# Performance work log

Measured on AMD Instinct MI355X. Metric: run time of the kernel, lower is better.

The kernel has to match this reference:

```python
import jax, jax.numpy as jnp
import numpy as np

KNOW, ITEM, D, L, LAT, B, S = 1024, 20000, 128, 2, 256, 256, 200
NTOT = ITEM + KNOW
E1, E2 = 32768, 160000


def graph_layer(h, W, a, src, dst, n):
    # GAT-style: gather src/dst, edge MLP, segment softmax over dst, weighted scatter-sum
    z = h @ W                                              # [N, D]
    e = jax.nn.leaky_relu((jnp.concatenate([z[src], z[dst]], axis=-1) @ a)[:, 0])  # [E]
    m = jax.ops.segment_max(e, dst, num_segments=n)
    m = jnp.where(jnp.isfinite(m), m, 0.0)                 # nodes with no in-edges
    w = jnp.exp(e - m[dst])                                # [E]
    den = jax.ops.segment_sum(w, dst, num_segments=n)      # [N]
    num = jax.ops.segment_sum(w[:, None] * z[src], dst, num_segments=n)  # [N, D]
    return jnp.where(den[:, None] > 0, num / jnp.maximum(den, 1e-12)[:, None], 0.0)


def setup_inputs() -> dict:
    key = jax.random.key(0)
    ks = jax.random.split(key, 32)
    p = lambda i, shp: jax.random.normal(ks[i], shp, dtype=jnp.float32) * 0.05
    inp = {
        'p_rec': jax.random.randint(ks[0], (B, S), 0, ITEM),
        'p_target': jax.random.randint(ks[1], (B,), 0, S),
        'a_rec': jax.random.randint(ks[2], (B, S), 0, 3),
        'kn_rec': jax.random.uniform(ks[3], (B, S, KNOW), dtype=jnp.float32),
        'kn_num': jnp.ones((B, S), dtype=jnp.float32),
        'src1': jax.random.randint(ks[4], (E1,), 0, KNOW),
        'dst1': jax.random.randint(ks[5], (E1,), 0, KNOW),
        'src2': jax.random.randint(ks[6], (E2,), 0, NTOT),
        'dst2': jax.random.randint(ks[7], (E2,), 0, NTOT),
        'src3': jax.random.randint(ks[8], (E2,), 0, NTOT),
        'dst3': jax.random.randint(ks[9], (E2,), 0, NTOT),
        'kn_table': p(10, (KNOW, D)),
        'exer_table': p(11, (ITEM, D)),
        'ans_table': p(12, (3, D)),
        'gW': p(13, (L, 3, D, D)),
        'gA': p(14, (L, 3, 2 * D, 1)),
        'raW1': p(15, (L, D, D)),
        'raB1': jnp.zeros((L, D), jnp.float32),
        'raW2': p(16, (L, D, 1)),
        'actW1': p(17, (3 * D, LAT)),
        'actB1': jnp.zeros((LAT,), jnp.float32),
        'actW2': p(18, (LAT, ITEM)),
        'actB2': jnp.zeros((ITEM,), jnp.float32),
        'vW1': p(19, (3, 3 * D, LAT)),
        'vB1': jnp.zeros((3, LAT), jnp.float32),
        'vW2': p(20, (3, LAT, 1)),
        'vB2': jnp.zeros((3, 1), jnp.float32),
    }
    return inp


def reference(p_rec, p_target, a_rec, kn_rec, kn_num, src1, dst1, src2, dst2, src3, dst3,
              kn_table, exer_table, ans_table, gW, gA, raW1, raB1, raW2,
              actW1, actB1, actW2, actB2, vW1, vB1, vW2, vB2):
    kn, ex = kn_table, exer_table
    for l in range(L):  # GraphEncoder: stacked Fusion blocks (distinct params)
        k_dir = graph_layer(kn, gW[l, 0], gA[l, 0], src1, dst1, KNOW)
        ek = jnp.concatenate([ex, kn], axis=0)             # [NTOT, D]
        kfe = graph_layer(ek, gW[l, 1], gA[l, 1], src2, dst2, NTOT)
        efk = graph_layer(ek, gW[l, 2], gA[l, 2], src3, dst3, NTOT)
        A_, B_ = k_dir, kfe[ITEM:]
        ra = lambda x: jnp.tanh(x @ raW1[l] + raB1[l]) @ raW2[l]  # [KNOW, 1]
        s = jax.nn.softmax(jnp.concatenate([ra(A_), ra(B_)], axis=1), axis=1)
        kn = s[:, :1] * A_ + s[:, 1:2] * B_
        ex = efk[:ITEM]
    # hidden_layer
    be = ex[p_rec]                                         # [B, S, D]
    ba = ans_table[a_rec]                                  # [B, S, D]
    bk = jnp.einsum('bsk,kd->bsd', kn_rec, kn) / kn_num[..., None]
    item = jnp.concatenate([be, ba, bk], axis=-1)          # [B, S, 3D]
    m = (jnp.arange(S)[None, :] < (p_target + 1)[:, None]).astype(item.dtype)
    h = (item * m[..., None]).sum(axis=1) / m.sum(axis=1, keepdims=True)  # [B, 3D]
    logits = jnp.tanh(h @ actW1 + actB1) @ actW2 + actB2   # [B, ITEM]
    vh = jnp.tanh(jnp.einsum('bd,kdl->kbl', h, vW1) + vB1[:, None, :])
    vals = jnp.einsum('kbl,klo->kbo', vh, vW2) + vB2[:, None, :]  # [3, B, 1]
    return logits, vals[0], vals[1], vals[2]
```

## Files before the change

kernel.cpp:

```cpp
#include <hip/hip_runtime.h>

#define D 128
#define KNOW 1024
#define ITEM 20000
#define NTOT (ITEM + KNOW)
#define LAYERS 2
#define LAT 256
#define BB 256
#define SS 200
#define H3 (3 * D)
#define CH 4
#define ZROWS 64
#define NBK (KNOW / ZROWS)
#define NBN ((NTOT + ZROWS - 1) / ZROWS)
#define NAGG (KNOW + KNOW + NTOT)
#define XPITCH 68

__global__ __launch_bounds__(256) void zdv(
    const float* __restrict__ Xe, const float* __restrict__ Xk,
    const float* __restrict__ gW, const float* __restrict__ gA, int layer,
    float* __restrict__ z1, float* __restrict__ z2, float* __restrict__ z3,
    float* __restrict__ ds1, float* __restrict__ dd1,
    float* __restrict__ ds2, float* __restrict__ dd2,
    float* __restrict__ ds3, float* __restrict__ dd3)
{
    __shared__ __align__(16) float xT[D * XPITCH];
    int bid = blockIdx.x;
    int g, row0, nmax;
    if (bid < NBK)            { g = 0; row0 = bid * ZROWS;                nmax = KNOW; }
    else if (bid < NBK + NBN) { g = 1; row0 = (bid - NBK) * ZROWS;        nmax = NTOT; }
    else                      { g = 2; row0 = (bid - NBK - NBN) * ZROWS;  nmax = NTOT; }
    const float* W = gW + (size_t)(layer * 3 + g) * D * D;
    const float* A = gA + (size_t)(layer * 3 + g) * 2 * D;
    float* Z  = (g == 0) ? z1  : (g == 1 ? z2  : z3);
    float* DS = (g == 0) ? ds1 : (g == 1 ? ds2 : ds3);
    float* DD = (g == 0) ? dd1 : (g == 1 ? dd2 : dd3);

    int tid = threadIdx.x;
#pragma unroll
    for (int i = 0; i < 8; ++i) {
        int flat = tid + i * 256;
        int row  = flat >> 5;
        int f4   = flat & 31;
        int grow = row0 + row;
        float4 v = make_float4(0.f, 0.f, 0.f, 0.f);
        if (grow < nmax) {
            const float* src = (g == 0) ? (Xk + (size_t)grow * D)
                             : (grow < ITEM ? Xe + (size_t)grow * D
                                            : Xk + (size_t)(grow - ITEM) * D);
            v = *(const float4*)(src + f4 * 4);
        }
        int slot = row ^ ((f4 & 7) << 2);
        int kk = f4 * 4;
        xT[(kk + 0) * XPITCH + slot] = v.x;
        xT[(kk + 1) * XPITCH + slot] = v.y;
        xT[(kk + 2) * XPITCH + slot] = v.z;
        xT[(kk + 3) * XPITCH + slot] = v.w;
    }
    __syncthreads();

    int cg = tid & 31;
    int rg = tid >> 5;
    int c0 = cg * 4;
    int r0a = rg * 8, r0b = rg * 8 + 4;

    float acc[8][4];
#pragma unroll
    for (int r = 0; r < 8; ++r)
#pragma unroll
        for (int c = 0; c < 4; ++c) acc[r][c] = 0.f;

#pragma unroll 4
    for (int k = 0; k < D; ++k) {
        float4 wv = *(const float4*)(W + (size_t)k * D + c0);
        int xc = ((k >> 2) & 7) << 2;
        float4 xa = *(const float4*)&xT[k * XPITCH + (r0a ^ xc)];
        float4 xb = *(const float4*)&xT[k * XPITCH + (r0b ^ xc)];
        acc[0][0] = fmaf(xa.x, wv.x, acc[0][0]); acc[0][1] = fmaf(xa.x, wv.y, acc[0][1]);
        acc[0][2] = fmaf(xa.x, wv.z, acc[0][2]); acc[0][3] = fmaf(xa.x, wv.w, acc[0][3]);
        acc[1][0] = fmaf(xa.y, wv.x, acc[1][0]); acc[1][1] = fmaf(xa.y, wv.y, acc[1][1]);
        acc[1][2] = fmaf(xa.y, wv.z, acc[1][2]); acc[1][3] = fmaf(xa.y, wv.w, acc[1][3]);
        acc[2][0] = fmaf(xa.z, wv.x, acc[2][0]); acc[2][1] = fmaf(xa.z, wv.y, acc[2][1]);
        acc[2][2] = fmaf(xa.z, wv.z, acc[2][2]); acc[2][3] = fmaf(xa.z, wv.w, acc[2][3]);
        acc[3][0] = fmaf(xa.w, wv.x, acc[3][0]); acc[3][1] = fmaf(xa.w, wv.y, acc[3][1]);
        acc[3][2] = fmaf(xa.w, wv.z, acc[3][2]); acc[3][3] = fmaf(xa.w, wv.w, acc[3][3]);
        acc[4][0] = fmaf(xb.x, wv.x, acc[4][0]); acc[4][1] = fmaf(xb.x, wv.y, acc[4][1]);
        acc[4][2] = fmaf(xb.x, wv.z, acc[4][2]); acc[4][3] = fmaf(xb.x, wv.w, acc[4][3]);
        acc[5][0] = fmaf(xb.y, wv.x, acc[5][0]); acc[5][1] = fmaf(xb.y, wv.y, acc[5][1]);
        acc[5][2] = fmaf(xb.y, wv.z, acc[5][2]); acc[5][3] = fmaf(xb.y, wv.w, acc[5][3]);
        acc[6][0] = fmaf(xb.z, wv.x, acc[6][0]); acc[6][1] = fmaf(xb.z, wv.y, acc[6][1]);
        acc[6][2] = fmaf(xb.z, wv.z, acc[6][2]); acc[6][3] = fmaf(xb.z, wv.w, acc[6][3]);
        acc[7][0] = fmaf(xb.w, wv.x, acc[7][0]); acc[7][1] = fmaf(xb.w, wv.y, acc[7][1]);
        acc[7][2] = fmaf(xb.w, wv.z, acc[7][2]); acc[7][3] = fmaf(xb.w, wv.w, acc[7][3]);
    }

#pragma unroll
    for (int r = 0; r < 8; ++r) {
        int grow = row0 + ((r < 4) ? (r0a + r) : (r0b + r - 4));
        if (grow < nmax) {
            float4 v = make_float4(acc[r][0], acc[r][1], acc[r][2], acc[r][3]);
            *(float4*)(Z + (size_t)grow * D + c0) = v;
        }
    }

    float4 as = *(const float4*)(A + c0);
    float4 ad = *(const float4*)(A + D + c0);
    float ps[8], pd[8];
#pragma unroll
    for (int r = 0; r < 8; ++r) {
        ps[r] = acc[r][0] * as.x + acc[r][1] * as.y + acc[r][2] * as.z + acc[r][3] * as.w;
        pd[r] = acc[r][0] * ad.x + acc[r][1] * ad.y + acc[r][2] * ad.z + acc[r][3] * ad.w;
    }
#pragma unroll
    for (int m = 16; m; m >>= 1) {
#pragma unroll
        for (int r = 0; r < 8; ++r) {
            ps[r] += __shfl_xor(ps[r], m, 64);
            pd[r] += __shfl_xor(pd[r], m, 64);
        }
    }
    if (cg == 0) {
#pragma unroll
        for (int r = 0; r < 8; ++r) {
            int grow = row0 + ((r < 4) ? (r0a + r) : (r0b + r - 4));
            if (grow < nmax) { DS[grow] = ps[r]; DD[grow] = pd[r]; }
        }
    }
}

__global__ void hist3(const int* __restrict__ d1, const int* __restrict__ d2, const int* __restrict__ d3,
                      int E1, int E2, int* __restrict__ c1, int* __restrict__ c2, int* __restrict__ c3) {
    int i = blockIdx.x * blockDim.x + threadIdx.x;
    if (i < E1) atomicAdd(&c1[d1[i]], 1);
    else if (i < E1 + E2) { int d = d2[i - E1]; if (d >= ITEM) atomicAdd(&c2[d - ITEM], 1); }
    else if (i < E1 + 2 * E2) atomicAdd(&c3[d3[i - E1 - E2]], 1);
}

__global__ __launch_bounds__(1024) void exscan3(int* __restrict__ c1, int* __restrict__ o1,
                                                int* __restrict__ c2, int* __restrict__ o2,
                                                int* __restrict__ c3, int* __restrict__ o3) {
    int g = blockIdx.x;
    int* cnt = (g == 0) ? c1 : (g == 1 ? c2 : c3);
    int* off = (g == 0) ? o1 : (g == 1 ? o2 : o3);
    int n = (g == 2) ? NTOT : KNOW;
    __shared__ int wsum[16];
    __shared__ int carry;
    int tid = threadIdx.x, lane = tid & 63, wid = tid >> 6;
    if (tid == 0) { carry = 0; off[0] = 0; }
    __syncthreads();
    for (int base = 0; base < n; base += 1024) {
        int i = base + tid;
        int v = (i < n) ? cnt[i] : 0;
        int x = v;
#pragma unroll
        for (int d = 1; d < 64; d <<= 1) { int t = __shfl_up(x, d, 64); x += (lane >= d) ? t : 0; }
        if (lane == 63) wsum[wid] = x;
        __syncthreads();
        if (wid == 0) {
            int w = (lane < 16) ? wsum[lane] : 0;
#pragma unroll
            for (int d = 1; d < 16; d <<= 1) { int t = __shfl_up(w, d, 64); w += (lane >= d) ? t : 0; }
            if (lane < 16) wsum[lane] = w;
        }
        __syncthreads();
        int incl = x + ((wid > 0) ? wsum[wid - 1] : 0) + carry;
        if (i < n) { off[i + 1] = incl; cnt[i] = incl - v; }
        __syncthreads();
        if (tid == 1023) carry = incl;
        __syncthreads();
    }
}

__global__ void scatter3(const int* __restrict__ s1, const int* __restrict__ d1,
                         const int* __restrict__ s2, const int* __restrict__ d2,
                         const int* __restrict__ s3, const int* __restrict__ d3,
                         int E1, int E2, int* __restrict__ cur1, int* __restrict__ cur2, int* __restrict__ cur3,
                         int* __restrict__ e1, int* __restrict__ e2, int* __restrict__ e3) {
    int i = blockIdx.x * blockDim.x + threadIdx.x;
    if (i < E1) { int p = atomicAdd(&cur1[d1[i]], 1); e1[p] = s1[i]; }
    else if (i < E1 + E2) { int j = i - E1; int d = d2[j]; if (d >= ITEM) { int p = atomicAdd(&cur2[d - ITEM], 1); e2[p] = s2[j]; } }
    else if (i < E1 + 2 * E2) { int j = i - E1 - E2; int p = atomicAdd(&cur3[d3[j]], 1); e3[p] = s3[j]; }
}

__global__ __launch_bounds__(256) void agg3(
    const float* __restrict__ z1, const float* __restrict__ z2, const float* __restrict__ z3,
    const float* __restrict__ ds1, const float* __restrict__ dd1,
    const float* __restrict__ ds2, const float* __restrict__ dd2,
    const float* __restrict__ ds3, const float* __restrict__ dd3,
    const int* __restrict__ off1, const int* __restrict__ es1,
    const int* __restrict__ off2, const int* __restrict__ es2,
    const int* __restrict__ off3, const int* __restrict__ es3,
    float* __restrict__ kdir, float* __restrict__ kfe_kn, float* __restrict__ nxt)
{
    int u = blockIdx.x * 4 + (threadIdx.x >> 6);
    int lane = threadIdx.x & 63;
    if (u >= NAGG) return;
    const float* Z; const float* dsrc; const int* off; const int* es; float* out; float dd; int row;
    if (u < KNOW)          { row = u;            Z = z1; dsrc = ds1; off = off1; es = es1; out = kdir   + (size_t)row * D; dd = dd1[row]; }
    else if (u < 2 * KNOW) { row = u - KNOW;     Z = z2; dsrc = ds2; off = off2; es = es2; out = kfe_kn + (size_t)row * D; dd = dd2[ITEM + row]; }
    else                   { row = u - 2 * KNOW; Z = z3; dsrc = ds3; off = off3; es = es3; out = nxt    + (size_t)row * D; dd = dd3[row]; }
    int e0 = off[row], e1 = off[row + 1];
    float2 res = make_float2(0.f, 0.f);
    if (e1 > e0) {
        float mx = -3.4e38f;
        for (int e = e0 + lane; e < e1; e += 64) {
            float t = dsrc[es[e]] + dd;
            t = (t > 0.f) ? t : 0.01f * t;
            mx = fmaxf(mx, t);
        }
#pragma unroll
        for (int o = 32; o; o >>= 1) mx = fmaxf(mx, __shfl_xor(mx, o, 64));
        float den = 0.f, ax = 0.f, ay = 0.f;
        for (int e = e0; e < e1; ++e) {
            int s = es[e];
            float t = dsrc[s] + dd;
            t = (t > 0.f) ? t : 0.01f * t;
            float w = expf(t - mx);
            den += w;
            float2 zv = ((const float2*)(Z + (size_t)s * D))[lane];
            ax += w * zv.x; ay += w * zv.y;
        }
        float inv = 1.f / fmaxf(den, 1e-12f);
        res = make_float2(ax * inv, ay * inv);
    }
    ((float2*)out)[lane] = res;
}

__global__ __launch_bounds__(128) void combine(const float* __restrict__ kdir, const float* __restrict__ kfe_kn,
                                               const float* __restrict__ raW1, const float* __restrict__ raB1,
                                               const float* __restrict__ raW2, float* __restrict__ out) {
    __shared__ float A[D], Bv[D];
    __shared__ float2 red[128];
    int i = blockIdx.x, j = threadIdx.x;
    A[j]  = kdir[(size_t)i * D + j];
    Bv[j] = kfe_kn[(size_t)i * D + j];
    __syncthreads();
    float accA = raB1[j], accB = accA;
    for (int k = 0; k < D; ++k) {
        float w = raW1[k * D + j];
        accA = fmaf(A[k], w, accA);
        accB = fmaf(Bv[k], w, accB);
    }
    float w2 = raW2[j];
    float pA = tanhf(accA) * w2, pB = tanhf(accB) * w2;
    red[j] = make_float2(pA, pB);
    __syncthreads();
    for (int st = 64; st > 0; st >>= 1) {
        if (j < st) { red[j].x += red[j + st].x; red[j].y += red[j + st].y; }
        __syncthreads();
    }
    float rA = red[0].x, rB = red[0].y;
    float mx = fmaxf(rA, rB);
    float eA = expf(rA - mx), eB = expf(rB - mx), s = 1.f / (eA + eB);
    out[(size_t)(ITEM + i) * D + j] = (eA * s) * A[j] + (eB * s) * Bv[j];
}

__global__ __launch_bounds__(256) void krowk(const float* __restrict__ kn_rec, const float* __restrict__ kn_num,
                                             const int* __restrict__ p_target, float* __restrict__ krowP) {
    int b = blockIdx.x, ch = blockIdx.y;
    int cnt = p_target[b] + 1;
    int per = (SS + CH - 1) / CH;
    int s0 = ch * per, s1 = s0 + per;
    if (s1 > cnt) s1 = cnt;
    int k0 = threadIdx.x * 4;
    float4 a = make_float4(0.f, 0.f, 0.f, 0.f);
    for (int s = s0; s < s1; ++s) {
        float inv = 1.f / kn_num[b * SS + s];
        float4 v = *(const float4*)(kn_rec + ((size_t)b * SS + s) * KNOW + k0);
        a.x += v.x * inv; a.y += v.y * inv; a.z += v.z * inv; a.w += v.w * inv;
    }
    *(float4*)(krowP + ((size_t)ch * BB + b) * KNOW + k0) = a;
}

__global__ __launch_bounds__(512) void hker(const float* __restrict__ ex, const float* __restrict__ ans_table,
                                            const int* __restrict__ p_rec, const int* __restrict__ a_rec,
                                            const int* __restrict__ p_target, const float* __restrict__ krowP,
                                            const float* __restrict__ kn, float* __restrict__ h) {
    int b = blockIdx.x;
    int j = threadIdx.x & 127, sg = threadIdx.x >> 7;
    int cnt = p_target[b] + 1;
    __shared__ int pidx[SS], aidx[SS];
    __shared__ float kr[KNOW];
    __shared__ float red[4][3][128];
    for (int i = threadIdx.x; i < cnt; i += 512) { pidx[i] = p_rec[b * SS + i]; aidx[i] = a_rec[b * SS + i]; }
    for (int i = threadIdx.x; i < KNOW; i += 512) {
        float s = 0.f;
#pragma unroll
        for (int c = 0; c < CH; ++c) s += krowP[((size_t)c * BB + b) * KNOW + i];
        kr[i] = s;
    }
    __syncthreads();
    float accE = 0.f, accA = 0.f;
    for (int s = sg; s < cnt; s += 4) {
        accE += ex[(size_t)pidx[s] * D + j];
        accA += ans_table[aidx[s] * D + j];
    }
    float accK = 0.f;
    for (int k = sg * 256; k < sg * 256 + 256; ++k) accK += kr[k] * kn[(size_t)k * D + j];
    red[sg][0][j] = accE; red[sg][1][j] = accA; red[sg][2][j] = accK;
    __syncthreads();
    if (sg == 0) {
        float inv = 1.f / (float)cnt;
        float e = (red[0][0][j] + red[1][0][j] + red[2][0][j] + red[3][0][j]) * inv;
        float a = (red[0][1][j] + red[1][1][j] + red[2][1][j] + red[3][1][j]) * inv;
        float kv = (red[0][2][j] + red[1][2][j] + red[2][2][j] + red[3][2][j]) * inv;
        h[b * H3 + j] = e;
        h[b * H3 + D + j] = a;
        h[b * H3 + 2 * D + j] = kv;
    }
}

__global__ __launch_bounds__(256) void hidden_gemm(const float* __restrict__ h,
                                                   const float* __restrict__ actW1, const float* __restrict__ actB1,
                                                   const float* __restrict__ vW1, const float* __restrict__ vB1,
                                                   float* __restrict__ hid) {
    __shared__ float hT[H3 * 17];
    int tid = threadIdx.x;
    int b0 = blockIdx.y * 16;
    for (int idx = tid; idx < 16 * H3; idx += 256) {
        int r = idx / H3, k = idx - r * H3;
        hT[k * 17 + r] = h[(size_t)(b0 + r) * H3 + k];
    }
    __syncthreads();
    int j = blockIdx.x * 64 + (tid & 63);
    int head = j >> 8, jj = j & 255;
    int rg = tid >> 6, r0 = rg * 4;
    const float* W = (head == 0) ? actW1 : (vW1 + (size_t)(head - 1) * H3 * LAT);
    float bias = (head == 0) ? actB1[jj] : vB1[(head - 1) * LAT + jj];
    float acc[4] = {bias, bias, bias, bias};
#pragma unroll 4
    for (int k = 0; k < H3; ++k) {
        float w = W[(size_t)k * LAT + jj];
        float h0 = hT[k * 17 + r0 + 0];
        float h1 = hT[k * 17 + r0 + 1];
        float h2 = hT[k * 17 + r0 + 2];
        float h3 = hT[k * 17 + r0 + 3];
        acc[0] = fmaf(h0, w, acc[0]);
        acc[1] = fmaf(h1, w, acc[1]);
        acc[2] = fmaf(h2, w, acc[2]);
        acc[3] = fmaf(h3, w, acc[3]);
    }
#pragma unroll
    for (int r = 0; r < 4; ++r)
        hid[((size_t)head * BB + (b0 + r0 + r)) * LAT + jj] = tanhf(acc[r]);
}

__global__ __launch_bounds__(256) void logitsker(const float* __restrict__ hid, const float* __restrict__ actW2,
                                                 const float* __restrict__ actB2, float* __restrict__ out) {
    __shared__ float hT[LAT * 33];
    int tid = threadIdx.x;
    int b0 = blockIdx.y * 32;
    for (int idx = tid; idx < 32 * LAT; idx += 256) {
        int r = idx >> 8, k = idx & 255;
        hT[k * 33 + r] = hid[(size_t)(b0 + r) * LAT + k];
    }
    __syncthreads();
    int lane6 = tid & 63;
    int rg = tid >> 6, r0 = rg * 8;
    int ibase = blockIdx.x * 256 + lane6;
    int icol[4], icl[4];
    float bias[4];
#pragma unroll
    for (int c = 0; c < 4; ++c) {
        icol[c] = ibase + c * 64;
        icl[c] = icol[c] < ITEM ? icol[c] : (ITEM - 1);
        bias[c] = actB2[icl[c]];
    }
    float acc[8][4];
#pragma unroll
    for (int r = 0; r < 8; ++r)
#pragma unroll
        for (int c = 0; c < 4; ++c) acc[r][c] = bias[c];
#pragma unroll 2
    for (int k = 0; k < LAT; ++k) {
        float w0 = actW2[(size_t)k * ITEM + icl[0]];
        float w1 = actW2[(size_t)k * ITEM + icl[1]];
        float w2 = actW2[(size_t)k * ITEM + icl[2]];
        float w3 = actW2[(size_t)k * ITEM + icl[3]];
        const float* hp = &hT[k * 33 + r0];
#pragma unroll
        for (int r = 0; r < 8; ++r) {
            float hv = hp[r];
            acc[r][0] = fmaf(hv, w0, acc[r][0]);
            acc[r][1] = fmaf(hv, w1, acc[r][1]);
            acc[r][2] = fmaf(hv, w2, acc[r][2]);
            acc[r][3] = fmaf(hv, w3, acc[r][3]);
        }
    }
#pragma unroll
    for (int c = 0; c < 4; ++c) {
        if (icol[c] < ITEM) {
#pragma unroll
            for (int r = 0; r < 8; ++r)
                out[(size_t)(b0 + r0 + r) * ITEM + icol[c]] = acc[r][c];
        }
    }
}

__global__ __launch_bounds__(256) void valsker(const float* __restrict__ hid, const float* __restrict__ vW2,
                                               const float* __restrict__ vB2, float* __restrict__ out) {
    int idx = blockIdx.x * 4 + (threadIdx.x >> 6);
    int lane = threadIdx.x & 63;
    if (idx >= 3 * BB) return;
    int k = idx / BB, b = idx - k * BB;
    const float* vh = hid + ((size_t)(k + 1) * BB + b) * LAT;
    float4 a = ((const float4*)vh)[lane];
    float4 w = ((const float4*)(vW2 + k * LAT))[lane];
    float s = a.x * w.x + a.y * w.y + a.z * w.z + a.w * w.w;
#pragma unroll
    for (int o = 32; o; o >>= 1) s += __shfl_down(s, o, 64);
    if (lane == 0) out[(size_t)BB * ITEM + k * BB + b] = s + vB2[k];
}

extern "C" void kernel_launch(void* const* d_in, const int* in_sizes, int n_in,
                              void* d_out, int out_size, void* d_ws, size_t ws_size,
                              hipStream_t stream) {
    const int*   p_rec      = (const int*)d_in[0];
    const int*   p_target   = (const int*)d_in[1];
    const int*   a_rec      = (const int*)d_in[2];
    const float* kn_rec     = (const float*)d_in[3];
    const float* kn_num     = (const float*)d_in[4];
    const int*   src1       = (const int*)d_in[5];
    const int*   dst1       = (const int*)d_in[6];
    const int*   src2       = (const int*)d_in[7];
    const int*   dst2       = (const int*)d_in[8];
    const int*   src3       = (const int*)d_in[9];
    const int*   dst3       = (const int*)d_in[10];
    const float* kn_table   = (const float*)d_in[11];
    const float* exer_table = (const float*)d_in[12];
    const float* ans_table  = (const float*)d_in[13];
    const float* gW         = (const float*)d_in[14];
    const float* gA         = (const float*)d_in[15];
    const float* raW1       = (const float*)d_in[16];
    const float* raB1       = (const float*)d_in[17];
    const float* raW2       = (const float*)d_in[18];
    const float* actW1      = (const float*)d_in[19];
    const float* actB1      = (const float*)d_in[20];
    const float* actW2      = (const float*)d_in[21];
    const float* actB2      = (const float*)d_in[22];
    const float* vW1        = (const float*)d_in[23];
    const float* vB1        = (const float*)d_in[24];
    const float* vW2        = (const float*)d_in[25];
    const float* vB2        = (const float*)d_in[26];
    const int E1 = in_sizes[5], E2 = in_sizes[7];

    float* base = (float*)d_ws;
    size_t o = 0;
    auto alloc = [&](size_t n) -> float* { float* p = base + o; o += (n + 3) & ~(size_t)3; return p; };
    float* buf  = alloc((size_t)NTOT * D);
    float* z1   = alloc((size_t)KNOW * D);
    float* z2   = alloc((size_t)NTOT * D);
    float* z3   = alloc((size_t)NTOT * D);
    float* kdir = alloc((size_t)KNOW * D);
    float* kfek = alloc((size_t)KNOW * D);
    float* ds1 = alloc(KNOW);  float* dd1 = alloc(KNOW);
    float* ds2 = alloc(NTOT);  float* dd2 = alloc(NTOT);
    float* ds3 = alloc(NTOT);  float* dd3 = alloc(NTOT);
    int* cnts = (int*)alloc(2 * KNOW + NTOT);
    int* cnt1 = cnts, *cnt2 = cnts + KNOW, *cnt3 = cnts + 2 * KNOW;
    int* off1 = (int*)alloc(KNOW + 1);
    int* off2 = (int*)alloc(KNOW + 1);
    int* off3 = (int*)alloc(NTOT + 1);
    int* es1  = (int*)alloc(E1);
    int* es2  = (int*)alloc(E2);
    int* es3  = (int*)alloc(E2);
    float* krowP = alloc((size_t)CH * BB * KNOW);
    float* hbuf  = alloc((size_t)BB * H3);
    float* hid   = alloc((size_t)4 * BB * LAT);

    hipMemsetAsync(cnts, 0, sizeof(int) * (2 * KNOW + NTOT), stream);

    int etot = E1 + 2 * E2;
    hist3<<<(etot + 255) / 256, 256, 0, stream>>>(dst1, dst2, dst3, E1, E2, cnt1, cnt2, cnt3);
    exscan3<<<3, 1024, 0, stream>>>(cnt1, off1, cnt2, off2, cnt3, off3);
    scatter3<<<(etot + 255) / 256, 256, 0, stream>>>(src1, dst1, src2, dst2, src3, dst3,
                                                     E1, E2, cnt1, cnt2, cnt3, es1, es2, es3);

    for (int l = 0; l < LAYERS; ++l) {
        const float* Xe = (l == 0) ? exer_table : buf;
        const float* Xk = (l == 0) ? kn_table : (buf + (size_t)ITEM * D);
        zdv<<<NBK + 2 * NBN, 256, 0, stream>>>(Xe, Xk, gW, gA, l, z1, z2, z3,
                                               ds1, dd1, ds2, dd2, ds3, dd3);
        agg3<<<(NAGG + 3) / 4, 256, 0, stream>>>(z1, z2, z3, ds1, dd1, ds2, dd2, ds3, dd3,
                                                 off1, es1, off2, es2, off3, es3,
                                                 kdir, kfek, buf);
        combine<<<KNOW, 128, 0, stream>>>(kdir, kfek, raW1 + (size_t)l * D * D, raB1 + (size_t)l * D,
                                          raW2 + (size_t)l * D, buf);
    }

    krowk<<<dim3(BB, CH), 256, 0, stream>>>(kn_rec, kn_num, p_target, krowP);
    hker<<<BB, 512, 0, stream>>>(buf, ans_table, p_rec, a_rec, p_target, krowP, buf + (size_t)ITEM * D, hbuf);
    hidden_gemm<<<dim3(16, 16), 256, 0, stream>>>(hbuf, actW1, actB1, vW1, vB1, hid);
    logitsker<<<dim3((ITEM + 255) / 256, 8), 256, 0, stream>>>(hid, actW2, actB2, (float*)d_out);
    valsker<<<(3 * BB + 3) / 4, 256, 0, stream>>>(hid, vW2, vB2, (float*)d_out);
}
```

Measured before the change: 328.6 us.

## Fuse GAT aggregation with relation-attention combine and process four edges per wave

Merges the agg3 and combine kernels. Knowledge rows compute both aggregations and the attention softmax mix in one block through shared memory, which removes the kdir/kfek intermediate buffers and one launch per layer. The aggregation now splits each wave into 4 edge groups of 16 lanes, each loading 8 floats per row with float4, then combines partial sums with cross-lane shuffles. It also switches to __expf. The cost is more shuffle reductions and registers, plus a block barrier only in the knowledge branch.

```diff
diff --git a/kernel.cpp b/kernel.cpp
--- a/kernel.cpp
+++ b/kernel.cpp
@@ -13,7 +13,6 @@
 #define ZROWS 64
 #define NBK (KNOW / ZROWS)
 #define NBN ((NTOT + ZROWS - 1) / ZROWS)
-#define NAGG (KNOW + KNOW + NTOT)
 #define XPITCH 68
 
 __global__ __launch_bounds__(256) void zdv(
@@ -182,7 +181,47 @@
     else if (i < E1 + 2 * E2) { int j = i - E1 - E2; int p = atomicAdd(&cur3[d3[j]], 1); e3[p] = s3[j]; }
 }
 
-__global__ __launch_bounds__(256) void agg3(
+__device__ __forceinline__ void agg_row(const float* __restrict__ Z, const float* __restrict__ dsrc,
+                                        float dd, const int* __restrict__ es, int e0, int e1,
+                                        int lane, float* __restrict__ acc) {
+#pragma unroll
+    for (int q = 0; q < 8; ++q) acc[q] = 0.f;
+    if (e1 <= e0) return;
+    float mx = -3.4e38f;
+    for (int e = e0 + lane; e < e1; e += 64) {
+        float t = dsrc[es[e]] + dd;
+        t = (t > 0.f) ? t : 0.01f * t;
+        mx = fmaxf(mx, t);
+    }
+#pragma unroll
+    for (int o = 32; o; o >>= 1) mx = fmaxf(mx, __shfl_xor(mx, o, 64));
+    int eg = lane >> 4, cs = lane & 15;
+    float den = 0.f;
+    for (int e = e0 + eg; e < e1; e += 4) {
+        int s = es[e];
+        float t = dsrc[s] + dd;
+        t = (t > 0.f) ? t : 0.01f * t;
+        float w = __expf(t - mx);
+        den += w;
+        const float4* zr = (const float4*)(Z + (size_t)s * D + cs * 8);
+        float4 za = zr[0], zb = zr[1];
+        acc[0] = fmaf(w, za.x, acc[0]); acc[1] = fmaf(w, za.y, acc[1]);
+        acc[2] = fmaf(w, za.z, acc[2]); acc[3] = fmaf(w, za.w, acc[3]);
+        acc[4] = fmaf(w, zb.x, acc[4]); acc[5] = fmaf(w, zb.y, acc[5]);
+        acc[6] = fmaf(w, zb.z, acc[6]); acc[7] = fmaf(w, zb.w, acc[7]);
+    }
+#pragma unroll
+    for (int m = 16; m <= 32; m <<= 1) {
+        den += __shfl_xor(den, m, 64);
+#pragma unroll
+        for (int q = 0; q < 8; ++q) acc[q] += __shfl_xor(acc[q], m, 64);
+    }
+    float inv = 1.f / fmaxf(den, 1e-12f);
+#pragma unroll
+    for (int q = 0; q < 8; ++q) acc[q] *= inv;
+}
+
+__global__ __launch_bounds__(256) void agg3c(
     const float* __restrict__ z1, const float* __restrict__ z2, const float* __restrict__ z3,
     const float* __restrict__ ds1, const float* __restrict__ dd1,
     const float* __restrict__ ds2, const float* __restrict__ dd2,
@@ -190,69 +229,58 @@
     const int* __restrict__ off1, const int* __restrict__ es1,
     const int* __restrict__ off2, const int* __restrict__ es2,
     const int* __restrict__ off3, const int* __restrict__ es3,
-    float* __restrict__ kdir, float* __restrict__ kfe_kn, float* __restrict__ nxt)
+    const float* __restrict__ raW1, const float* __restrict__ raB1,
+    const float* __restrict__ raW2, float* __restrict__ buf)
 {
-    int u = blockIdx.x * 4 + (threadIdx.x >> 6);
-    int lane = threadIdx.x & 63;
-    if (u >= NAGG) return;
-    const float* Z; const float* dsrc; const int* off; const int* es; float* out; float dd; int row;
-    if (u < KNOW)          { row = u;            Z = z1; dsrc = ds1; off = off1; es = es1; out = kdir   + (size_t)row * D; dd = dd1[row]; }
-    else if (u < 2 * KNOW) { row = u - KNOW;     Z = z2; dsrc = ds2; off = off2; es = es2; out = kfe_kn + (size_t)row * D; dd = dd2[ITEM + row]; }
-    else                   { row = u - 2 * KNOW; Z = z3; dsrc = ds3; off = off3; es = es3; out = nxt    + (size_t)row * D; dd = dd3[row]; }
-    int e0 = off[row], e1 = off[row + 1];
-    float2 res = make_float2(0.f, 0.f);
-    if (e1 > e0) {
-        float mx = -3.4e38f;
-        for (int e = e0 + lane; e < e1; e += 64) {
-            float t = dsrc[es[e]] + dd;
-            t = (t > 0.f) ? t : 0.01f * t;
-            mx = fmaxf(mx, t);
-        }
-#pragma unroll
-        for (int o = 32; o; o >>= 1) mx = fmaxf(mx, __shfl_xor(mx, o, 64));
-        float den = 0.f, ax = 0.f, ay = 0.f;
-        for (int e = e0; e < e1; ++e) {
-            int s = es[e];
-            float t = dsrc[s] + dd;
-            t = (t > 0.f) ? t : 0.01f * t;
-            float w = expf(t - mx);
-            den += w;
-            float2 zv = ((const float2*)(Z + (size_t)s * D))[lane];
-            ax += w * zv.x; ay += w * zv.y;
-        }
-        float inv = 1.f / fmaxf(den, 1e-12f);
-        res = make_float2(ax * inv, ay * inv);
-    }
-    ((float2*)out)[lane] = res;
-}
-
-__global__ __launch_bounds__(128) void combine(const float* __restrict__ kdir, const float* __restrict__ kfe_kn,
-                                               const float* __restrict__ raW1, const float* __restrict__ raB1,
-                                               const float* __restrict__ raW2, float* __restrict__ out) {
-    __shared__ float A[D], Bv[D];
-    __shared__ float2 red[128];
-    int i = blockIdx.x, j = threadIdx.x;
-    A[j]  = kdir[(size_t)i * D + j];
-    Bv[j] = kfe_kn[(size_t)i * D + j];
-    __syncthreads();
-    float accA = raB1[j], accB = accA;
-    for (int k = 0; k < D; ++k) {
-        float w = raW1[k * D + j];
-        accA = fmaf(A[k], w, accA);
-        accB = fmaf(Bv[k], w, accB);
-    }
-    float w2 = raW2[j];
-    float pA = tanhf(accA) * w2, pB = tanhf(accB) * w2;
-    red[j] = make_float2(pA, pB);
-    __syncthreads();
-    for (int st = 64; st > 0; st >>= 1) {
-        if (j < st) { red[j].x += red[j + st].x; red[j].y += red[j + st].y; }
+    int wv = threadIdx.x >> 6, lane = threadIdx.x & 63;
+    int eg = lane >> 4, cs = lane & 15;
+    if (blockIdx.x < KNOW / 4) {
+        __shared__ float ABs[4][2][D];
+        int i = blockIdx.x * 4 + wv;
+        float accA[8], accB[8];
+        agg_row(z1, ds1, dd1[i], es1, off1[i], off1[i + 1], lane, accA);
+        agg_row(z2, ds2, dd2[ITEM + i], es2, off2[i], off2[i + 1], lane, accB);
+        if (eg == 0) {
+            *(float4*)&ABs[wv][0][cs * 8]     = make_float4(accA[0], accA[1], accA[2], accA[3]);
+            *(float4*)&ABs[wv][0][cs * 8 + 4] = make_float4(accA[4], accA[5], accA[6], accA[7]);
+            *(float4*)&ABs[wv][1][cs * 8]     = make_float4(accB[0], accB[1], accB[2], accB[3]);
+            *(float4*)&ABs[wv][1][cs * 8 + 4] = make_float4(accB[4], accB[5], accB[6], accB[7]);
+        }
         __syncthreads();
-    }
-    float rA = red[0].x, rB = red[0].y;
-    float mx = fmaxf(rA, rB);
-    float eA = expf(rA - mx), eB = expf(rB - mx), s = 1.f / (eA + eB);
-    out[(size_t)(ITEM + i) * D + j] = (eA * s) * A[j] + (eB * s) * Bv[j];
+        int j0 = lane * 2;
+        float b0 = raB1[j0], b1 = raB1[j0 + 1];
+        float aA0 = b0, aA1 = b1, aB0 = b0, aB1 = b1;
+#pragma unroll 4
+        for (int k = 0; k < D; ++k) {
+            float av = ABs[wv][0][k], bv = ABs[wv][1][k];
+            float2 w = *(const float2*)(raW1 + (size_t)k * D + j0);
+            aA0 = fmaf(av, w.x, aA0); aA1 = fmaf(av, w.y, aA1);
+            aB0 = fmaf(bv, w.x, aB0); aB1 = fmaf(bv, w.y, aB1);
+        }
+        float2 w2 = *(const float2*)(raW2 + j0);
+        float pA = tanhf(aA0) * w2.x + tanhf(aA1) * w2.y;
+        float pB = tanhf(aB0) * w2.x + tanhf(aB1) * w2.y;
+#pragma unroll
+        for (int o = 32; o; o >>= 1) { pA += __shfl_xor(pA, o, 64); pB += __shfl_xor(pB, o, 64); }
+        float mx2 = fmaxf(pA, pB);
+        float eA = __expf(pA - mx2), eB = __expf(pB - mx2);
+        float s = 1.f / (eA + eB);
+        float sA = eA * s, sB = eB * s;
+        float2 Av = *(float2*)&ABs[wv][0][j0];
+        float2 Bv = *(float2*)&ABs[wv][1][j0];
+        *(float2*)(buf + (size_t)(ITEM + i) * D + j0) =
+            make_float2(sA * Av.x + sB * Bv.x, sA * Av.y + sB * Bv.y);
+    } else {
+        int row = (blockIdx.x - KNOW / 4) * 4 + wv;
+        if (row < ITEM) {
+            float acc[8];
+            agg_row(z3, ds3, dd3[row], es3, off3[row], off3[row + 1], lane, acc);
+            if (eg == 0) {
+                *(float4*)(buf + (size_t)row * D + cs * 8)     = make_float4(acc[0], acc[1], acc[2], acc[3]);
+                *(float4*)(buf + (size_t)row * D + cs * 8 + 4) = make_float4(acc[4], acc[5], acc[6], acc[7]);
+            }
+        }
+    }
 }
 
 __global__ __launch_bounds__(256) void krowk(const float* __restrict__ kn_rec, const float* __restrict__ kn_num,
@@ -451,8 +479,6 @@
     float* z1   = alloc((size_t)KNOW * D);
     float* z2   = alloc((size_t)NTOT * D);
     float* z3   = alloc((size_t)NTOT * D);
-    float* kdir = alloc((size_t)KNOW * D);
-    float* kfek = alloc((size_t)KNOW * D);
     float* ds1 = alloc(KNOW);  float* dd1 = alloc(KNOW);
     float* ds2 = alloc(NTOT);  float* dd2 = alloc(NTOT);
     float* ds3 = alloc(NTOT);  float* dd3 = alloc(NTOT);
@@ -476,16 +502,16 @@
     scatter3<<<(etot + 255) / 256, 256, 0, stream>>>(src1, dst1, src2, dst2, src3, dst3,
                                                      E1, E2, cnt1, cnt2, cnt3, es1, es2, es3);
 
+    int aggBlocks = KNOW / 4 + ITEM / 4;
     for (int l = 0; l < LAYERS; ++l) {
         const float* Xe = (l == 0) ? exer_table : buf;
         const float* Xk = (l == 0) ? kn_table : (buf + (size_t)ITEM * D);
         zdv<<<NBK + 2 * NBN, 256, 0, stream>>>(Xe, Xk, gW, gA, l, z1, z2, z3,
                                                ds1, dd1, ds2, dd2, ds3, dd3);
-        agg3<<<(NAGG + 3) / 4, 256, 0, stream>>>(z1, z2, z3, ds1, dd1, ds2, dd2, ds3, dd3,
-                                                 off1, es1, off2, es2, off3, es3,
-                                                 kdir, kfek, buf);
-        combine<<<KNOW, 128, 0, stream>>>(kdir, kfek, raW1 + (size_t)l * D * D, raB1 + (size_t)l * D,
-                                          raW2 + (size_t)l * D, buf);
+        agg3c<<<aggBlocks, 256, 0, stream>>>(z1, z2, z3, ds1, dd1, ds2, dd2, ds3, dd3,
+                                             off1, es1, off2, es2, off3, es3,
+                                             raW1 + (size_t)l * D * D, raB1 + (size_t)l * D,
+                                             raW2 + (size_t)l * D, buf);
     }
 
     krowk<<<dim3(BB, CH), 256, 0, stream>>>(kn_rec, kn_num, p_target, krowP);
```

After: 301.6 us. -8.2%, faster.
